# Performance work log

Hardware: AMD Instinct MI355X
Metric: run time of the kernel (lower is better)

Reference implementation:

```python
import jax, jax.numpy as jnp
import numpy as np

B, T, D = 2, 2048, 1024
H = 16
DH = D // H
SCALE = DH ** -0.5


def setup_inputs() -> dict:
    key = jax.random.key(0)
    ks = jax.random.split(key, 9)
    s = D ** -0.5
    return {
        "x": jax.random.normal(ks[0], (B, T, D), dtype=jnp.float32),
        "Wq": jax.random.normal(ks[1], (D, D), dtype=jnp.float32) * s,
        "bq": jax.random.normal(ks[2], (D,), dtype=jnp.float32) * 0.01,
        "Wk": jax.random.normal(ks[3], (D, D), dtype=jnp.float32) * s,
        "bk": jax.random.normal(ks[4], (D,), dtype=jnp.float32) * 0.01,
        "Wv": jax.random.normal(ks[5], (D, D), dtype=jnp.float32) * s,
        "bv": jax.random.normal(ks[6], (D,), dtype=jnp.float32) * 0.01,
        "Wo": jax.random.normal(ks[7], (D, D), dtype=jnp.float32) * s,
        "bo": jax.random.normal(ks[8], (D,), dtype=jnp.float32) * 0.01,
    }


def reference(x, Wq, bq, Wk, bk, Wv, bv, Wo, bo):
    # projections; torch Linear: y = x @ W.T + b. Here W is stored as (in, out).
    q = (x @ Wq + bq).reshape(B, T, H, DH).transpose(0, 2, 1, 3)  # (B,H,T,DH)
    k = (x @ Wk + bk).reshape(B, T, H, DH).transpose(0, 2, 1, 3)
    v = (x @ Wv + bv).reshape(B, T, H, DH).transpose(0, 2, 1, 3)
    scores = jnp.einsum("bhqd,bhkd->bhqk", q, k) * SCALE  # (B,H,T,T)
    causal = jnp.tril(jnp.ones((T, T), dtype=bool))
    scores = jnp.where(causal, scores, -jnp.inf)
    probs = jax.nn.softmax(scores, axis=-1)
    out = jnp.einsum("bhqk,bhkd->bhqd", probs, v)  # (B,H,T,DH)
    out = out.transpose(0, 2, 1, 3).reshape(B, T, D)
    out = out @ Wo + bo
    return out, (k, v)
```

## Files before the change

### kernel.cpp

```cpp
#include <hip/hip_runtime.h>

typedef float  f32x4  __attribute__((ext_vector_type(4)));
typedef float  f32x16 __attribute__((ext_vector_type(16)));
typedef __bf16 bf16x8 __attribute__((ext_vector_type(8)));
typedef short  s16x8  __attribute__((ext_vector_type(8)));
typedef short  s16x4  __attribute__((ext_vector_type(4)));
typedef unsigned int u32x4 __attribute__((ext_vector_type(4)));

static __device__ __forceinline__ unsigned short f2bf(float f) {
  return __builtin_bit_cast(unsigned short, (__bf16)f);
}
static __device__ __forceinline__ bf16x8 bc8(s16x8 v) {
  return __builtin_bit_cast(bf16x8, v);
}
static __device__ __forceinline__ f32x16 mfma32(bf16x8 a, bf16x8 b, f32x16 c) {
  return __builtin_amdgcn_mfma_f32_32x32x16_bf16(a, b, c, 0, 0, 0);
}
static __device__ __forceinline__ f32x4 mfma16(bf16x8 a, bf16x8 b, f32x4 c) {
  return __builtin_amdgcn_mfma_f32_16x16x32_bf16(a, b, c, 0, 0, 0);
}

static __device__ __forceinline__ void gl2lds16(const unsigned short* g, unsigned short* l) {
  __builtin_amdgcn_global_load_lds(
      (const __attribute__((address_space(1))) unsigned int*)g,
      (__attribute__((address_space(3))) unsigned int*)l, 16, 0, 0);
}

#define GSYNC(NSTR)                                          \
  do {                                                       \
    __builtin_amdgcn_sched_barrier(0);                       \
    asm volatile("s_waitcnt vmcnt(" NSTR ")" ::: "memory");  \
    __builtin_amdgcn_s_barrier();                            \
    __builtin_amdgcn_sched_barrier(0);                       \
  } while (0)

__global__ void prep_k(const float* __restrict__ x, unsigned short* __restrict__ xb,
                       const float* __restrict__ W0, const float* __restrict__ W1,
                       const float* __restrict__ W2, const float* __restrict__ W3,
                       unsigned short* __restrict__ wtb) {
  __shared__ unsigned short tl[64][72];
  const int bid = blockIdx.x;
  const int t = threadIdx.x;
  if (bid < 2048) {
    int i = (bid * 256 + t) * 8;
    float4 a = *(const float4*)(x + i);
    float4 b = *(const float4*)(x + i + 4);
    s16x8 o;
    o[0] = (short)f2bf(a.x); o[1] = (short)f2bf(a.y);
    o[2] = (short)f2bf(a.z); o[3] = (short)f2bf(a.w);
    o[4] = (short)f2bf(b.x); o[5] = (short)f2bf(b.y);
    o[6] = (short)f2bf(b.z); o[7] = (short)f2bf(b.w);
    *(s16x8*)(xb + i) = o;
    return;
  }
  const int rid = bid - 2048;
  const int z = rid >> 8, rem = rid & 255;
  const float* W = z == 0 ? W0 : z == 1 ? W1 : z == 2 ? W2 : W3;
  unsigned short* out = wtb + (size_t)z * 1048576;
  const int nt = (rem & 15) * 64, kt = (rem >> 4) * 64;
  const int row = t >> 2, seg = t & 3;
  const float* src = W + (kt + row) * 1024 + nt + seg * 16;
#pragma unroll
  for (int q = 0; q < 4; ++q) {
    float4 v = *(const float4*)(src + q * 4);
    tl[seg * 16 + q * 4 + 0][row] = f2bf(v.x);
    tl[seg * 16 + q * 4 + 1][row] = f2bf(v.y);
    tl[seg * 16 + q * 4 + 2][row] = f2bf(v.z);
    tl[seg * 16 + q * 4 + 3][row] = f2bf(v.w);
  }
  __syncthreads();
  unsigned short* dst = out + (nt + row) * 1024 + kt + seg * 16;
  *(s16x8*)dst       = *(const s16x8*)&tl[row][seg * 16];
  *(s16x8*)(dst + 8) = *(const s16x8*)&tl[row][seg * 16 + 8];
}

static __device__ __forceinline__ int trans_ix(int m, int n) {
  int b = m >> 11, tt = m & 2047, h = n >> 6, dh = n & 63;
  return ((b << 4) + h) * 131072 + tt * 64 + dh;
}

__global__ __launch_bounds__(512, 4) void gemm_qkv_k(const unsigned short* __restrict__ A,
                                                     const unsigned short* __restrict__ BT,
                                                     const float* __restrict__ b0,
                                                     const float* __restrict__ b1,
                                                     const float* __restrict__ b2,
                                                     float* __restrict__ outF,
                                                     unsigned short* __restrict__ oq,
                                                     unsigned short* __restrict__ ok,
                                                     unsigned short* __restrict__ ovT) {
  extern __shared__ unsigned short lds[];
  const int t = threadIdx.x;
  const int lane = t & 63, ln = lane & 15, g = lane >> 4;
  const int w = t >> 6, wm = w >> 2, wn = w & 3;
  const unsigned wgid = blockIdx.x;
  const unsigned swz = (wgid & 7) * 64 + (wgid >> 3);
  const int by = swz & 31, bx = swz >> 5;
  const int bm0 = by * 128, bn0 = bx * 192;

  const int ar = t >> 2;
  const unsigned short* aBase = A + (size_t)(bm0 + ar) * 1024 + (((t & 3) ^ ((ar >> 1) & 3)) * 8);
  const int br = t >> 3;
  const int bcol = (t & 7) ^ (br & 7);
  const unsigned short* bBase = BT + (size_t)(bn0 + br) * 1024 + bcol * 8;

  auto issueA = [&](int buf, int H, int kt) {
    gl2lds16(aBase + kt + H * 32, &lds[buf * 20480 + H * 4096 + t * 8]);
  };
  auto issueB = [&](int buf, int j, int kt) {
    gl2lds16(bBase + (size_t)j * 65536 + kt, &lds[buf * 20480 + 8192 + j * 4096 + t * 8]);
  };
  auto ldA = [&](int buf, int H, int mf) -> bf16x8 {
    const int row = wm * 64 + mf * 16 + ln;
    const int sp = g ^ ((row >> 1) & 3);
    return bc8(*(const s16x8*)&lds[buf * 20480 + H * 4096 + row * 32 + sp * 8]);
  };
  auto ldB = [&](int buf, int H, int nf) -> bf16x8 {
    const int row = wn * 48 + nf * 16 + ln;
    const int sp = (H * 4 + g) ^ (row & 7);
    return bc8(*(const s16x8*)&lds[buf * 20480 + 8192 + row * 64 + sp * 8]);
  };

  f32x4 acc[4][3] = {};
  issueA(0, 0, 0);
  issueB(0, 0, 0);
  issueB(0, 1, 0);
  issueB(0, 2, 0);
  issueA(0, 1, 0);

  for (int ti = 0; ti < 16; ++ti) {
    const int buf = ti & 1, nb = buf ^ 1;
    const bool hn = ti < 15;
    const int kn = (ti + 1) * 64;

    GSYNC("1");
    if (hn) { issueA(nb, 0, kn); issueB(nb, 0, kn); issueB(nb, 1, kn); }
    {
      bf16x8 afr[4], bfr[3];
#pragma unroll
      for (int mf = 0; mf < 4; ++mf) afr[mf] = ldA(buf, 0, mf);
#pragma unroll
      for (int nf = 0; nf < 3; ++nf) bfr[nf] = ldB(buf, 0, nf);
      __builtin_amdgcn_s_setprio(1);
#pragma unroll
      for (int mf = 0; mf < 4; ++mf)
#pragma unroll
        for (int nf = 0; nf < 3; ++nf) acc[mf][nf] = mfma16(afr[mf], bfr[nf], acc[mf][nf]);
      __builtin_amdgcn_s_setprio(0);
    }
    if (hn) GSYNC("3"); else GSYNC("0");
    if (hn) { issueB(nb, 2, kn); issueA(nb, 1, kn); }
    {
      bf16x8 afr[4], bfr[3];
#pragma unroll
      for (int mf = 0; mf < 4; ++mf) afr[mf] = ldA(buf, 1, mf);
#pragma unroll
      for (int nf = 0; nf < 3; ++nf) bfr[nf] = ldB(buf, 1, nf);
      __builtin_amdgcn_s_setprio(1);
#pragma unroll
      for (int mf = 0; mf < 4; ++mf)
#pragma unroll
        for (int nf = 0; nf < 3; ++nf) acc[mf][nf] = mfma16(afr[mf], bfr[nf], acc[mf][nf]);
      __builtin_amdgcn_s_setprio(0);
    }
  }

#pragma unroll
  for (int nf = 0; nf < 3; ++nf) {
    const int n = bn0 + wn * 48 + nf * 16 + ln;
    const int n1 = n & 1023;
    const float* bp = n < 1024 ? b0 : (n < 2048 ? b1 : b2);
    const float bias = bp[n1];
    if (n < 1024) {
#pragma unroll
      for (int mf = 0; mf < 4; ++mf)
#pragma unroll
        for (int r = 0; r < 4; ++r) {
          const int m = bm0 + wm * 64 + mf * 16 + g * 4 + r;
          oq[trans_ix(m, n1)] = f2bf((acc[mf][nf][r] + bias) * 0.18033688f);
        }
    } else if (n < 2048) {
#pragma unroll
      for (int mf = 0; mf < 4; ++mf)
#pragma unroll
        for (int r = 0; r < 4; ++r) {
          const int m = bm0 + wm * 64 + mf * 16 + g * 4 + r;
          const float v = acc[mf][nf][r] + bias;
          const int ix = trans_ix(m, n1);
          ok[ix] = f2bf(v);
          outF[4194304 + ix] = v;
        }
    } else {
      const int dh = n1 & 63, hh = n1 >> 6;
#pragma unroll
      for (int mf = 0; mf < 4; ++mf) {
        const int m0 = bm0 + wm * 64 + mf * 16 + g * 4;
        const int bb = m0 >> 11, tt = m0 & 2047;
        s16x4 pv;
#pragma unroll
        for (int r = 0; r < 4; ++r) {
          const float v = acc[mf][nf][r] + bias;
          outF[8388608 + trans_ix(m0 + r, n1)] = v;
          pv[r] = (short)f2bf(v);
        }
        *(s16x4*)(ovT + (size_t)((bb << 4) + hh) * 131072 + (size_t)dh * 2048 + tt) = pv;
      }
    }
  }
}

__global__ __launch_bounds__(512, 4) void gemm_o_k(const unsigned short* __restrict__ A,
                                                   const unsigned short* __restrict__ BT,
                                                   const float* __restrict__ b0,
                                                   float* __restrict__ outF) {
  extern __shared__ unsigned short lds[];
  const int t = threadIdx.x;
  const int lane = t & 63, ln = lane & 15, g = lane >> 4;
  const int w = t >> 6, wm = w >> 2, wn = w & 3;
  const unsigned wgid = blockIdx.x;
  const unsigned swz = (wgid & 7) * 64 + (wgid >> 3);
  const int bx = swz & 7, by = swz >> 3;
  const int bm0 = by * 64, bn0 = bx * 128;

  const int row = t >> 3;
  const int scol = (t & 7) ^ (row & 7);
  const unsigned short* aSrc = A + (size_t)(bm0 + row) * 1024 + scol * 8;
  const unsigned short* bSrc0 = BT + (size_t)(bn0 + row) * 1024 + scol * 8;
  const unsigned short* bSrc1 = BT + (size_t)(bn0 + 64 + row) * 1024 + scol * 8;

  auto issue3 = [&](int buf, int ti) {
    const int kt = ti * 64;
    gl2lds16(aSrc + kt, &lds[buf * 12288 + t * 8]);
    gl2lds16(bSrc0 + kt, &lds[buf * 12288 + 4096 + t * 8]);
    gl2lds16(bSrc1 + kt, &lds[buf * 12288 + 8192 + t * 8]);
  };
  auto ldA = [&](int buf, int H, int mf) -> bf16x8 {
    const int r = wm * 32 + mf * 16 + ln;
    const int sp = (H * 4 + g) ^ (r & 7);
    return bc8(*(const s16x8*)&lds[buf * 12288 + r * 64 + sp * 8]);
  };
  auto ldB = [&](int buf, int H, int nf) -> bf16x8 {
    const int r = wn * 32 + nf * 16 + ln;
    const int j = r >> 6, rl = r & 63;
    const int sp = (H * 4 + g) ^ (rl & 7);
    return bc8(*(const s16x8*)&lds[buf * 12288 + 4096 + j * 4096 + rl * 64 + sp * 8]);
  };

  f32x4 acc[2][2] = {};
  issue3(0, 0);
  issue3(1, 1);

  for (int i = 0; i < 16; ++i) {
    const int buf = i & 1;
    if (i < 15) GSYNC("3"); else GSYNC("0");
    bf16x8 a0[2], a1[2], bq0[2], bq1[2];
#pragma unroll
    for (int mf = 0; mf < 2; ++mf) { a0[mf] = ldA(buf, 0, mf); a1[mf] = ldA(buf, 1, mf); }
#pragma unroll
    for (int nf = 0; nf < 2; ++nf) { bq0[nf] = ldB(buf, 0, nf); bq1[nf] = ldB(buf, 1, nf); }
    asm volatile("s_waitcnt lgkmcnt(0)" ::: "memory");
    __builtin_amdgcn_sched_barrier(0);
    __builtin_amdgcn_s_barrier();
    __builtin_amdgcn_sched_barrier(0);
    if (i + 2 < 16) issue3(buf, i + 2);
    __builtin_amdgcn_s_setprio(1);
#pragma unroll
    for (int mf = 0; mf < 2; ++mf)
#pragma unroll
      for (int nf = 0; nf < 2; ++nf) {
        acc[mf][nf] = mfma16(a0[mf], bq0[nf], acc[mf][nf]);
        acc[mf][nf] = mfma16(a1[mf], bq1[nf], acc[mf][nf]);
      }
    __builtin_amdgcn_s_setprio(0);
  }

#pragma unroll
  for (int nf = 0; nf < 2; ++nf) {
    const int n = bn0 + wn * 32 + nf * 16 + ln;
    const float bias = b0[n];
#pragma unroll
    for (int mf = 0; mf < 2; ++mf)
#pragma unroll
      for (int r = 0; r < 4; ++r) {
        const int m = bm0 + wm * 32 + mf * 16 + g * 4 + r;
        outF[(size_t)m * 1024 + n] = acc[mf][nf][r] + bias;
      }
  }
}

__global__ __launch_bounds__(768) void attn_k(const unsigned short* __restrict__ qb,
                                              const unsigned short* __restrict__ kb,
                                              const unsigned short* __restrict__ vbT,
                                              unsigned short* __restrict__ ob) {
  extern __shared__ s16x8 kvS[];
  const int t = threadIdx.x;
  const int lane = t & 63, l31 = lane & 31, h5 = lane >> 5;
  const int w = t >> 6, grp = w >> 2, qw = w & 3;
  const unsigned wg = blockIdx.x;
  const int x = wg & 7, r_ = wg >> 3;
  const int bh = x + 8 * (r_ >> 3);
  const int p = r_ & 7;
  const int b = bh >> 4, h = bh & 15;
  const unsigned short* Qp = qb + (size_t)bh * 131072;
  const unsigned short* Kp = kb + (size_t)bh * 131072;
  const unsigned short* Vp = vbT + (size_t)bh * 131072;

  const int e0 = t & 255;
  const int kr0 = e0 >> 3;
  const int kcol = (e0 & 7) ^ (kr0 & 7);
  const unsigned short* kSrc = Kp + (size_t)kr0 * 64 + kcol * 8;
  const unsigned short* vSrc = Vp + (size_t)kr0 * 2048 + kcol * 8;
  s16x8* gB = &kvS[grp * 3072];

  s16x8 onesv;
#pragma unroll
  for (int z = 0; z < 8; ++z) onesv[z] = (short)0x3F80;
  const bf16x8 onesf = bc8(onesv);

  float* sc = (float*)kvS;
  const int slot = qw * 64 + lane;

  for (int half = 0; half < 2; ++half) {
    const int qblk = half == 0 ? p : 15 - p;
    const int q0 = qblk * 128;
    const int N64 = 2 * qblk + 2;
    const int base = N64 / 3, rem3 = N64 % 3;
    const int cnt = base + (grp < rem3 ? 1 : 0);
    const int start = grp * base + (grp < rem3 ? grp : rem3);
    const int NP = base + (rem3 ? 1 : 0);
    const int qg = q0 + qw * 32 + l31;

    __syncthreads();

    bf16x8 qf[4];
#pragma unroll
    for (int m = 0; m < 4; ++m)
      qf[m] = bc8(*(const s16x8*)(Qp + (size_t)qg * 64 + 16 * m + 8 * h5));

    auto issue = [&](int T, int buf) {
      const int kv0 = T * 64;
      unsigned short* kd = (unsigned short*)&gB[buf * 1024];
      unsigned short* vd = (unsigned short*)&gB[buf * 1024 + 512];
      const unsigned short* ks = kSrc + (size_t)kv0 * 64;
      const unsigned short* vs = vSrc + kv0;
      gl2lds16(ks,         kd + e0 * 8);
      gl2lds16(ks + 2048,  kd + (e0 + 256) * 8);
      gl2lds16(vs,         vd + e0 * 8);
      gl2lds16(vs + 65536, vd + (e0 + 256) * 8);
    };

    if (cnt > 0) issue(start, 0);
    if (cnt > 1) issue(start + 1, 1);

    f32x16 o0 = {}, o1 = {}, lsum = {};

    for (int i = 0; i < NP; ++i) {
      __builtin_amdgcn_sched_barrier(0);
      if (i + 1 < cnt) asm volatile("s_waitcnt vmcnt(4)" ::: "memory");
      else             asm volatile("s_waitcnt vmcnt(0)" ::: "memory");
      __builtin_amdgcn_s_barrier();
      __builtin_amdgcn_sched_barrier(0);
      if (i + 2 < cnt) issue(start + i + 2, (i + 2) % 3);
      const int T = start + i;
      const int kv0 = T * 64;
      const bool active = (i < cnt) && (kv0 <= q0 + qw * 32 + 31);
      if (active) {
        const int buf = i % 3;
        const s16x8* kb_ = &gB[buf * 1024];
        const s16x8* vb2 = &gB[buf * 1024 + 512];
        f32x16 s0 = {}, s1 = {};
        __builtin_amdgcn_s_setprio(1);
#pragma unroll
        for (int m = 0; m < 4; ++m) {
          const int sl = 2 * m + h5;
          bf16x8 a0 = bc8(kb_[l31 * 8 + (sl ^ (l31 & 7))]);
          bf16x8 a1 = bc8(kb_[(l31 + 32) * 8 + (sl ^ (l31 & 7))]);
          s0 = mfma32(a0, qf[m], s0);
          s1 = mfma32(a1, qf[m], s1);
        }
        __builtin_amdgcn_s_setprio(0);
        if (kv0 + 63 > q0 + qw * 32) {
#pragma unroll
          for (int r = 0; r < 16; ++r) {
            const int kvr = kv0 + (r & 3) + 8 * (r >> 2) + 4 * h5;
            if (kvr > qg) s0[r] = -1e30f;
            if (kvr + 32 > qg) s1[r] = -1e30f;
          }
        }
#pragma unroll
        for (int r = 0; r < 16; ++r) {
          s0[r] = __builtin_amdgcn_exp2f(s0[r]);
          s1[r] = __builtin_amdgcn_exp2f(s1[r]);
        }
        unsigned og[2][4][2];
#pragma unroll
        for (int gg = 0; gg < 4; ++gg) {
          asm("v_cvt_pk_bf16_f32 %0, %1, %2" : "=v"(og[0][gg][0]) : "v"(s0[4 * gg]),     "v"(s0[4 * gg + 1]));
          asm("v_cvt_pk_bf16_f32 %0, %1, %2" : "=v"(og[0][gg][1]) : "v"(s0[4 * gg + 2]), "v"(s0[4 * gg + 3]));
          asm("v_cvt_pk_bf16_f32 %0, %1, %2" : "=v"(og[1][gg][0]) : "v"(s1[4 * gg]),     "v"(s1[4 * gg + 1]));
          asm("v_cvt_pk_bf16_f32 %0, %1, %2" : "=v"(og[1][gg][1]) : "v"(s1[4 * gg + 2]), "v"(s1[4 * gg + 3]));
        }
        bf16x8 pf[4];
#pragma unroll
        for (int mp = 0; mp < 4; ++mp) {
          const int tau = mp >> 1, lc = mp & 1;
          unsigned a0 = og[tau][2 * lc][0], bq0 = og[tau][2 * lc + 1][0];
          unsigned a1 = og[tau][2 * lc][1], bq1 = og[tau][2 * lc + 1][1];
          asm volatile("v_permlane32_swap_b32 %0, %1" : "+v"(a0), "+v"(bq0));
          asm volatile("v_permlane32_swap_b32 %0, %1" : "+v"(a1), "+v"(bq1));
          u32x4 fw; fw[0] = a0; fw[1] = a1; fw[2] = bq0; fw[3] = bq1;
          pf[mp] = __builtin_bit_cast(bf16x8, fw);
        }
        __builtin_amdgcn_s_setprio(1);
#pragma unroll
        for (int mp = 0; mp < 4; ++mp) {
          const int sl = 2 * mp + h5;
          bf16x8 va0 = bc8(vb2[l31 * 8 + (sl ^ (l31 & 7))]);
          bf16x8 va1 = bc8(vb2[(l31 + 32) * 8 + (sl ^ (l31 & 7))]);
          o0 = mfma32(va0, pf[mp], o0);
          o1 = mfma32(va1, pf[mp], o1);
          lsum = mfma32(onesf, pf[mp], lsum);
        }
        __builtin_amdgcn_s_setprio(0);
      }
    }

    __syncthreads();
    if (grp > 0) {
      float* dst = sc + (size_t)(grp - 1) * 8704 + (size_t)slot * 34;
#pragma unroll
      for (int r = 0; r < 8; ++r) {
        *(float2*)(dst + 2 * r)      = make_float2(o0[2 * r], o0[2 * r + 1]);
        *(float2*)(dst + 16 + 2 * r) = make_float2(o1[2 * r], o1[2 * r + 1]);
      }
      dst[32] = lsum[0];
    }
    __syncthreads();
    if (grp == 0) {
      const float* p0 = sc + (size_t)slot * 34;
      const float* p1 = p0 + 8704;
      const float inv = 1.0f / (lsum[0] + p0[32] + p1[32]);
      unsigned short* orow = ob + (size_t)(b * 2048 + qg) * 1024 + h * 64;
#pragma unroll
      for (int rq = 0; rq < 4; ++rq) {
        s16x4 ov0, ov1;
#pragma unroll
        for (int e = 0; e < 4; ++e) {
          const int ei = 4 * rq + e;
          ov0[e] = (short)f2bf((o0[ei] + p0[ei] + p1[ei]) * inv);
          ov1[e] = (short)f2bf((o1[ei] + p0[16 + ei] + p1[16 + ei]) * inv);
        }
        *(s16x4*)(orow + 8 * rq + 4 * h5)      = ov0;
        *(s16x4*)(orow + 32 + 8 * rq + 4 * h5) = ov1;
      }
    }
  }
}

extern "C" void kernel_launch(void* const* d_in, const int* in_sizes, int n_in,
                              void* d_out, int out_size, void* d_ws, size_t ws_size,
                              hipStream_t stream) {
  (void)in_sizes; (void)n_in; (void)out_size; (void)ws_size;
  const float* x  = (const float*)d_in[0];
  const float* Wq = (const float*)d_in[1];
  const float* bq = (const float*)d_in[2];
  const float* Wk = (const float*)d_in[3];
  const float* bk = (const float*)d_in[4];
  const float* Wv = (const float*)d_in[5];
  const float* bv = (const float*)d_in[6];
  const float* Wo = (const float*)d_in[7];
  const float* bo = (const float*)d_in[8];
  float* out = (float*)d_out;

  unsigned short* ws  = (unsigned short*)d_ws;
  unsigned short* xb  = ws;
  unsigned short* wtb = ws + 4194304;
  unsigned short* qbuf = ws + 8388608;
  unsigned short* kbuf = qbuf + 4194304;
  unsigned short* vbuf = kbuf + 4194304;
  unsigned short* ab   = vbuf + 4194304;

  prep_k<<<3072, 256, 0, stream>>>(x, xb, Wq, Wk, Wv, Wo, wtb);
  gemm_qkv_k<<<512, 512, 81920, stream>>>(xb, wtb, bq, bk, bv, out, qbuf, kbuf, vbuf);
  attn_k<<<256, 768, 147456, stream>>>(qbuf, kbuf, vbuf, ab);
  gemm_o_k<<<512, 512, 49152, stream>>>(ab, wtb + 3145728, bo, out);
}
```

Baseline: 93.86 us.

## Retile QKV GEMM to 128x128 tiles with triple-buffered K=32 pipeline

Shrinks the QKV projection GEMM tile from 128x192 to 128x128, which launches 768 workgroups instead of 512 and cuts LDS use per block to 48 KB. The K loop changes from a double-buffered 64-wide step split into halves to a triple-buffered 32-wide step that prefetches two stages ahead. The aim is more resident blocks per CU (launch bound raised to 6), better load balance across CUs, and deeper latency hiding. The cost is less data reuse per tile, more global and LDS traffic per FLOP, and twice as many barriers.

```diff
diff --git a/kernel.cpp b/kernel.cpp
--- a/kernel.cpp
+++ b/kernel.cpp
@@ -79,7 +79,7 @@
   return ((b << 4) + h) * 131072 + tt * 64 + dh;
 }
 
-__global__ __launch_bounds__(512, 4) void gemm_qkv_k(const unsigned short* __restrict__ A,
+__global__ __launch_bounds__(512, 6) void gemm_qkv_k(const unsigned short* __restrict__ A,
                                                      const unsigned short* __restrict__ BT,
                                                      const float* __restrict__ b0,
                                                      const float* __restrict__ b1,
@@ -93,80 +93,55 @@
   const int lane = t & 63, ln = lane & 15, g = lane >> 4;
   const int w = t >> 6, wm = w >> 2, wn = w & 3;
   const unsigned wgid = blockIdx.x;
-  const unsigned swz = (wgid & 7) * 64 + (wgid >> 3);
+  const unsigned swz = (wgid & 7) * 96 + (wgid >> 3);
   const int by = swz & 31, bx = swz >> 5;
-  const int bm0 = by * 128, bn0 = bx * 192;
+  const int bm0 = by * 128, bn0 = bx * 128;
 
   const int ar = t >> 2;
-  const unsigned short* aBase = A + (size_t)(bm0 + ar) * 1024 + (((t & 3) ^ ((ar >> 1) & 3)) * 8);
-  const int br = t >> 3;
-  const int bcol = (t & 7) ^ (br & 7);
-  const unsigned short* bBase = BT + (size_t)(bn0 + br) * 1024 + bcol * 8;
-
-  auto issueA = [&](int buf, int H, int kt) {
-    gl2lds16(aBase + kt + H * 32, &lds[buf * 20480 + H * 4096 + t * 8]);
-  };
-  auto issueB = [&](int buf, int j, int kt) {
-    gl2lds16(bBase + (size_t)j * 65536 + kt, &lds[buf * 20480 + 8192 + j * 4096 + t * 8]);
-  };
-  auto ldA = [&](int buf, int H, int mf) -> bf16x8 {
+  const int as = (t & 3) ^ (ar & 3);
+  const unsigned short* aBase = A + (size_t)(bm0 + ar) * 1024 + as * 8;
+  const unsigned short* bBase = BT + (size_t)(bn0 + ar) * 1024 + as * 8;
+
+  auto issue = [&](int T, int buf) {
+    const int kt = T * 32;
+    gl2lds16(aBase + kt, &lds[buf * 8192 + t * 8]);
+    gl2lds16(bBase + kt, &lds[buf * 8192 + 4096 + t * 8]);
+  };
+  auto ldA = [&](int buf, int mf) -> bf16x8 {
     const int row = wm * 64 + mf * 16 + ln;
-    const int sp = g ^ ((row >> 1) & 3);
-    return bc8(*(const s16x8*)&lds[buf * 20480 + H * 4096 + row * 32 + sp * 8]);
-  };
-  auto ldB = [&](int buf, int H, int nf) -> bf16x8 {
-    const int row = wn * 48 + nf * 16 + ln;
-    const int sp = (H * 4 + g) ^ (row & 7);
-    return bc8(*(const s16x8*)&lds[buf * 20480 + 8192 + row * 64 + sp * 8]);
-  };
-
-  f32x4 acc[4][3] = {};
-  issueA(0, 0, 0);
-  issueB(0, 0, 0);
-  issueB(0, 1, 0);
-  issueB(0, 2, 0);
-  issueA(0, 1, 0);
-
-  for (int ti = 0; ti < 16; ++ti) {
-    const int buf = ti & 1, nb = buf ^ 1;
-    const bool hn = ti < 15;
-    const int kn = (ti + 1) * 64;
-
-    GSYNC("1");
-    if (hn) { issueA(nb, 0, kn); issueB(nb, 0, kn); issueB(nb, 1, kn); }
-    {
-      bf16x8 afr[4], bfr[3];
-#pragma unroll
-      for (int mf = 0; mf < 4; ++mf) afr[mf] = ldA(buf, 0, mf);
-#pragma unroll
-      for (int nf = 0; nf < 3; ++nf) bfr[nf] = ldB(buf, 0, nf);
-      __builtin_amdgcn_s_setprio(1);
-#pragma unroll
-      for (int mf = 0; mf < 4; ++mf)
-#pragma unroll
-        for (int nf = 0; nf < 3; ++nf) acc[mf][nf] = mfma16(afr[mf], bfr[nf], acc[mf][nf]);
-      __builtin_amdgcn_s_setprio(0);
-    }
-    if (hn) GSYNC("3"); else GSYNC("0");
-    if (hn) { issueB(nb, 2, kn); issueA(nb, 1, kn); }
-    {
-      bf16x8 afr[4], bfr[3];
-#pragma unroll
-      for (int mf = 0; mf < 4; ++mf) afr[mf] = ldA(buf, 1, mf);
-#pragma unroll
-      for (int nf = 0; nf < 3; ++nf) bfr[nf] = ldB(buf, 1, nf);
-      __builtin_amdgcn_s_setprio(1);
-#pragma unroll
-      for (int mf = 0; mf < 4; ++mf)
-#pragma unroll
-        for (int nf = 0; nf < 3; ++nf) acc[mf][nf] = mfma16(afr[mf], bfr[nf], acc[mf][nf]);
-      __builtin_amdgcn_s_setprio(0);
-    }
-  }
-
-#pragma unroll
-  for (int nf = 0; nf < 3; ++nf) {
-    const int n = bn0 + wn * 48 + nf * 16 + ln;
+    const int sp = g ^ (row & 3);
+    return bc8(*(const s16x8*)&lds[buf * 8192 + row * 32 + sp * 8]);
+  };
+  auto ldB = [&](int buf, int nf) -> bf16x8 {
+    const int row = wn * 32 + nf * 16 + ln;
+    const int sp = g ^ (row & 3);
+    return bc8(*(const s16x8*)&lds[buf * 8192 + 4096 + row * 32 + sp * 8]);
+  };
+
+  f32x4 acc[4][2] = {};
+  issue(0, 0);
+  issue(1, 1);
+
+  for (int i = 0; i < 32; ++i) {
+    const int buf = i % 3;
+    if (i < 31) GSYNC("2"); else GSYNC("0");
+    if (i + 2 < 32) issue(i + 2, (i + 2) % 3);
+    bf16x8 af[4], bfr[2];
+#pragma unroll
+    for (int mf = 0; mf < 4; ++mf) af[mf] = ldA(buf, mf);
+#pragma unroll
+    for (int nf = 0; nf < 2; ++nf) bfr[nf] = ldB(buf, nf);
+    __builtin_amdgcn_s_setprio(1);
+#pragma unroll
+    for (int mf = 0; mf < 4; ++mf)
+#pragma unroll
+      for (int nf = 0; nf < 2; ++nf) acc[mf][nf] = mfma16(af[mf], bfr[nf], acc[mf][nf]);
+    __builtin_amdgcn_s_setprio(0);
+  }
+
+#pragma unroll
+  for (int nf = 0; nf < 2; ++nf) {
+    const int n = bn0 + wn * 32 + nf * 16 + ln;
     const int n1 = n & 1023;
     const float* bp = n < 1024 ? b0 : (n < 2048 ? b1 : b2);
     const float bias = bp[n1];
@@ -480,7 +455,7 @@
   unsigned short* ab   = vbuf + 4194304;
 
   prep_k<<<3072, 256, 0, stream>>>(x, xb, Wq, Wk, Wv, Wo, wtb);
-  gemm_qkv_k<<<512, 512, 81920, stream>>>(xb, wtb, bq, bk, bv, out, qbuf, kbuf, vbuf);
+  gemm_qkv_k<<<768, 512, 49152, stream>>>(xb, wtb, bq, bk, bv, out, qbuf, kbuf, vbuf);
   attn_k<<<256, 768, 147456, stream>>>(qbuf, kbuf, vbuf, ab);
   gemm_o_k<<<512, 512, 49152, stream>>>(ab, wtb + 3145728, bo, out);
 }
```

After: 107.0 us. +14.0%, slower.

## Enlarge QKV GEMM tile to 256x192 and restructure LDS staging schedule

Applied to the files above, without the earlier changes.

The QKV projection GEMM tile grows from 128x192 to 256x192, so each wave computes 8x3 MFMA fragments instead of 4x3 and B tiles are reused across twice as many rows. The grid halves to 256 workgroups, LDS per block grows to 112KB, and launch bounds drop to 2 blocks per CU. The global-to-LDS issue order is regrouped so all B loads go in the first half-step and all A loads in the second, with the wait counts adjusted to match. The larger tile cuts LDS and global traffic per FLOP but raises register pressure and lowers occupancy, and with 256 blocks the CUs may be underfilled.

```diff
diff --git a/kernel.cpp b/kernel.cpp
--- a/kernel.cpp
+++ b/kernel.cpp
@@ -79,7 +79,7 @@
   return ((b << 4) + h) * 131072 + tt * 64 + dh;
 }
 
-__global__ __launch_bounds__(512, 4) void gemm_qkv_k(const unsigned short* __restrict__ A,
+__global__ __launch_bounds__(512, 2) void gemm_qkv_k(const unsigned short* __restrict__ A,
                                                      const unsigned short* __restrict__ BT,
                                                      const float* __restrict__ b0,
                                                      const float* __restrict__ b1,
@@ -93,73 +93,79 @@
   const int lane = t & 63, ln = lane & 15, g = lane >> 4;
   const int w = t >> 6, wm = w >> 2, wn = w & 3;
   const unsigned wgid = blockIdx.x;
-  const unsigned swz = (wgid & 7) * 64 + (wgid >> 3);
-  const int by = swz & 31, bx = swz >> 5;
-  const int bm0 = by * 128, bn0 = bx * 192;
-
-  const int ar = t >> 2;
-  const unsigned short* aBase = A + (size_t)(bm0 + ar) * 1024 + (((t & 3) ^ ((ar >> 1) & 3)) * 8);
-  const int br = t >> 3;
-  const int bcol = (t & 7) ^ (br & 7);
-  const unsigned short* bBase = BT + (size_t)(bn0 + br) * 1024 + bcol * 8;
-
-  auto issueA = [&](int buf, int H, int kt) {
-    gl2lds16(aBase + kt + H * 32, &lds[buf * 20480 + H * 4096 + t * 8]);
-  };
-  auto issueB = [&](int buf, int j, int kt) {
-    gl2lds16(bBase + (size_t)j * 65536 + kt, &lds[buf * 20480 + 8192 + j * 4096 + t * 8]);
+  const unsigned swz = (wgid & 7) * 32 + (wgid >> 3);
+  const int by = swz & 15, bx = swz >> 4;
+  const int bm0 = by * 256, bn0 = bx * 192;
+
+  const int brow = t >> 3;
+  const unsigned short* bSrcBase =
+      BT + (size_t)(bn0 + brow) * 1024 + (((t & 7) ^ (brow & 7)) * 8);
+  const int arow = t >> 2;
+  const unsigned short* aSrcBase =
+      A + (size_t)(bm0 + arow) * 1024 + (((t & 3) ^ ((t >> 3) & 3)) * 8);
+
+  auto issueB = [&](int T, int buf) {
+    const int kt = T * 64;
+#pragma unroll
+    for (int j = 0; j < 3; ++j)
+      gl2lds16(bSrcBase + (size_t)j * 65536 + kt, &lds[buf * 28672 + j * 4096 + t * 8]);
+  };
+  auto issueA = [&](int T, int buf) {
+    const int kt = T * 64;
+#pragma unroll
+    for (int H = 0; H < 2; ++H)
+#pragma unroll
+      for (int a = 0; a < 2; ++a)
+        gl2lds16(aSrcBase + (size_t)a * 131072 + kt + H * 32,
+                 &lds[buf * 28672 + 12288 + H * 8192 + a * 4096 + t * 8]);
   };
   auto ldA = [&](int buf, int H, int mf) -> bf16x8 {
-    const int row = wm * 64 + mf * 16 + ln;
+    const int row = wm * 128 + mf * 16 + ln;
     const int sp = g ^ ((row >> 1) & 3);
-    return bc8(*(const s16x8*)&lds[buf * 20480 + H * 4096 + row * 32 + sp * 8]);
+    return bc8(*(const s16x8*)&lds[buf * 28672 + 12288 + H * 8192 + row * 32 + sp * 8]);
   };
   auto ldB = [&](int buf, int H, int nf) -> bf16x8 {
     const int row = wn * 48 + nf * 16 + ln;
     const int sp = (H * 4 + g) ^ (row & 7);
-    return bc8(*(const s16x8*)&lds[buf * 20480 + 8192 + row * 64 + sp * 8]);
-  };
-
-  f32x4 acc[4][3] = {};
-  issueA(0, 0, 0);
-  issueB(0, 0, 0);
-  issueB(0, 1, 0);
-  issueB(0, 2, 0);
-  issueA(0, 1, 0);
+    return bc8(*(const s16x8*)&lds[buf * 28672 + row * 64 + sp * 8]);
+  };
+
+  f32x4 acc[8][3] = {};
+  issueB(0, 0);
+  issueA(0, 0);
 
   for (int ti = 0; ti < 16; ++ti) {
     const int buf = ti & 1, nb = buf ^ 1;
     const bool hn = ti < 15;
-    const int kn = (ti + 1) * 64;
-
-    GSYNC("1");
-    if (hn) { issueA(nb, 0, kn); issueB(nb, 0, kn); issueB(nb, 1, kn); }
+
+    GSYNC("2");
+    if (hn) issueB(ti + 1, nb);
     {
-      bf16x8 afr[4], bfr[3];
-#pragma unroll
-      for (int mf = 0; mf < 4; ++mf) afr[mf] = ldA(buf, 0, mf);
+      bf16x8 af[8], bfr[3];
+#pragma unroll
+      for (int mf = 0; mf < 8; ++mf) af[mf] = ldA(buf, 0, mf);
 #pragma unroll
       for (int nf = 0; nf < 3; ++nf) bfr[nf] = ldB(buf, 0, nf);
       __builtin_amdgcn_s_setprio(1);
 #pragma unroll
-      for (int mf = 0; mf < 4; ++mf)
-#pragma unroll
-        for (int nf = 0; nf < 3; ++nf) acc[mf][nf] = mfma16(afr[mf], bfr[nf], acc[mf][nf]);
+      for (int mf = 0; mf < 8; ++mf)
+#pragma unroll
+        for (int nf = 0; nf < 3; ++nf) acc[mf][nf] = mfma16(af[mf], bfr[nf], acc[mf][nf]);
       __builtin_amdgcn_s_setprio(0);
     }
     if (hn) GSYNC("3"); else GSYNC("0");
-    if (hn) { issueB(nb, 2, kn); issueA(nb, 1, kn); }
+    if (hn) issueA(ti + 1, nb);
     {
-      bf16x8 afr[4], bfr[3];
-#pragma unroll
-      for (int mf = 0; mf < 4; ++mf) afr[mf] = ldA(buf, 1, mf);
+      bf16x8 af[8], bfr[3];
+#pragma unroll
+      for (int mf = 0; mf < 8; ++mf) af[mf] = ldA(buf, 1, mf);
 #pragma unroll
       for (int nf = 0; nf < 3; ++nf) bfr[nf] = ldB(buf, 1, nf);
       __builtin_amdgcn_s_setprio(1);
 #pragma unroll
-      for (int mf = 0; mf < 4; ++mf)
-#pragma unroll
-        for (int nf = 0; nf < 3; ++nf) acc[mf][nf] = mfma16(afr[mf], bfr[nf], acc[mf][nf]);
+      for (int mf = 0; mf < 8; ++mf)
+#pragma unroll
+        for (int nf = 0; nf < 3; ++nf) acc[mf][nf] = mfma16(af[mf], bfr[nf], acc[mf][nf]);
       __builtin_amdgcn_s_setprio(0);
     }
   }
@@ -172,18 +178,18 @@
     const float bias = bp[n1];
     if (n < 1024) {
 #pragma unroll
-      for (int mf = 0; mf < 4; ++mf)
+      for (int mf = 0; mf < 8; ++mf)
 #pragma unroll
         for (int r = 0; r < 4; ++r) {
-          const int m = bm0 + wm * 64 + mf * 16 + g * 4 + r;
+          const int m = bm0 + wm * 128 + mf * 16 + g * 4 + r;
           oq[trans_ix(m, n1)] = f2bf((acc[mf][nf][r] + bias) * 0.18033688f);
         }
     } else if (n < 2048) {
 #pragma unroll
-      for (int mf = 0; mf < 4; ++mf)
+      for (int mf = 0; mf < 8; ++mf)
 #pragma unroll
         for (int r = 0; r < 4; ++r) {
-          const int m = bm0 + wm * 64 + mf * 16 + g * 4 + r;
+          const int m = bm0 + wm * 128 + mf * 16 + g * 4 + r;
           const float v = acc[mf][nf][r] + bias;
           const int ix = trans_ix(m, n1);
           ok[ix] = f2bf(v);
@@ -192,8 +198,8 @@
     } else {
       const int dh = n1 & 63, hh = n1 >> 6;
 #pragma unroll
-      for (int mf = 0; mf < 4; ++mf) {
-        const int m0 = bm0 + wm * 64 + mf * 16 + g * 4;
+      for (int mf = 0; mf < 8; ++mf) {
+        const int m0 = bm0 + wm * 128 + mf * 16 + g * 4;
         const int bb = m0 >> 11, tt = m0 & 2047;
         s16x4 pv;
 #pragma unroll
@@ -480,7 +486,7 @@
   unsigned short* ab   = vbuf + 4194304;
 
   prep_k<<<3072, 256, 0, stream>>>(x, xb, Wq, Wk, Wv, Wo, wtb);
-  gemm_qkv_k<<<512, 512, 81920, stream>>>(xb, wtb, bq, bk, bv, out, qbuf, kbuf, vbuf);
+  gemm_qkv_k<<<256, 512, 114688, stream>>>(xb, wtb, bq, bk, bv, out, qbuf, kbuf, vbuf);
   attn_k<<<256, 768, 147456, stream>>>(qbuf, kbuf, vbuf, ab);
   gemm_o_k<<<512, 512, 49152, stream>>>(ab, wtb + 3145728, bo, out);
 }
```

Result: no change. 94.23 us (+0.4%).
